# Kernel tuning notes

Measured on AMD Instinct MI355X. Metric: run time of the kernel, lower is better.

Reference implementation:

```python
import jax, jax.numpy as jnp
import numpy as np

ITER_N = 3  # iterNum
DIM = 256   # channel dim entering MPNCOV
# static flat indices of the upper triangle (row-major of dim*dim), as in Triuvec
_TRIU_I, _TRIU_J = np.triu_indices(DIM)
TRIU_IDX = jnp.asarray(_TRIU_I * DIM + _TRIU_J)


def setup_inputs() -> dict:
    key = jax.random.key(0)
    x = jax.random.normal(key, (256, 256, 14, 14), dtype=jnp.float32)
    return {"x": x}


def reference(x):
    B, C, H, W = x.shape
    M = H * W
    xr = x.reshape(B, C, M)
    # Covpool: y = x @ I_hat @ x^T with I_hat = (1/M)(I - (1/M) 1 1^T)
    # equivalently (1/M) * centered Gram matrix
    xc = xr - xr.mean(axis=2, keepdims=True)
    cov = jnp.einsum('bcm,bdm->bcd', xc, xc) / M  # [B, C, C]
    # Sqrtm: Newton-Schulz iteration (iSQRT-COV)
    I = jnp.eye(C, dtype=x.dtype)
    normA = jnp.trace(cov, axis1=1, axis2=2)  # = (1/3)*sum(cov * 3I)
    A = cov / normA[:, None, None]
    ZY = 0.5 * (3.0 * I - A)
    Yk = jnp.matmul(A, ZY)
    Zk = ZY
    for _ in range(ITER_N - 2):
        ZY = 0.5 * (3.0 * I - jnp.matmul(Zk, Yk))
        Yk = jnp.matmul(Yk, ZY)
        Zk = jnp.matmul(ZY, Zk)
    YZY = 0.5 * jnp.matmul(Yk, 3.0 * I - jnp.matmul(Zk, Yk))
    y = YZY * jnp.sqrt(normA)[:, None, None]
    # Triuvec: extract upper-triangular entries, [B, C*(C+1)/2]
    return y.reshape(B, C * C)[:, TRIU_IDX]
```

## Files before the change

### kernel.cpp

```cpp
#include <hip/hip_runtime.h>
#include <math.h>

#define BB 256
#define CC 256
#define MN 196
#define TRI 32896

#define MSC 32.0f
#define INV_MSC  (1.0f/32.0f)
#define INV_MSC2 (1.0f/1024.0f)

typedef _Float16 f16;
typedef f16   f16x8 __attribute__((ext_vector_type(8)));
typedef float f32x4 __attribute__((ext_vector_type(4)));
typedef unsigned u32x4 __attribute__((ext_vector_type(4)));

__device__ __forceinline__ unsigned pack_split(float v) {
    f16 h = (f16)v;
    f16 l = (f16)(v - (float)h);
    return (unsigned)__builtin_bit_cast(unsigned short, h) |
           ((unsigned)__builtin_bit_cast(unsigned short, l) << 16);
}
__device__ __forceinline__ float unpack_split(unsigned w) {
    f16 h = __builtin_bit_cast(f16, (unsigned short)(w & 0xffffu));
    f16 l = __builtin_bit_cast(f16, (unsigned short)(w >> 16));
    return (float)h + (float)l;
}
__device__ __forceinline__ f16x8 swap_pairs(f16x8 v) {
    return __builtin_shufflevector(v, v, 1, 0, 3, 2, 5, 4, 7, 6);
}
__device__ __forceinline__ void gload_lds16(const unsigned* g, const f16* l) {
    __builtin_amdgcn_global_load_lds(
        (__attribute__((address_space(1))) void*)(size_t)g,
        (__attribute__((address_space(3))) void*)(unsigned)(size_t)l,
        16, 0, 0);
}

__global__ __launch_bounds__(256) void xsplit_kernel(const float* __restrict__ x,
                                                     float* __restrict__ vr,
                                                     unsigned* __restrict__ xs, int b0) {
    int wave = (blockIdx.x * 256 + threadIdx.x) >> 6;
    int lane = threadIdx.x & 63;
    int bl = wave >> 8;
    int c  = wave & 255;
    int bg = b0 + bl;
    const float* row = x + ((size_t)bg * CC + c) * MN;
    float a0 = row[lane], a1 = row[lane + 64], a2 = row[lane + 128];
    float a3 = (lane < MN - 192) ? row[lane + 192] : 0.0f;
    float s = a0 + a1 + a2 + a3;
    float q = a0 * a0 + a1 * a1 + a2 * a2 + a3 * a3;
    #pragma unroll
    for (int off = 32; off > 0; off >>= 1) {
        s += __shfl_xor(s, off, 64);
        q += __shfl_xor(q, off, 64);
    }
    float m = s * (1.0f / MN);
    if (lane == 0) vr[bg * CC + c] = q * (1.0f / MN) - m * m;
    unsigned* orow = xs + ((size_t)bl * CC + c) * 256;
    orow[lane]       = pack_split(MSC * (a0 - m));
    orow[lane + 64]  = pack_split(MSC * (a1 - m));
    orow[lane + 128] = pack_split(MSC * (a2 - m));
    orow[lane + 192] = (lane < 4) ? pack_split(MSC * (a3 - m)) : 0u;
}

__global__ __launch_bounds__(256) void norm_kernel(const float* __restrict__ vr,
                                                   float* __restrict__ inv,
                                                   float* __restrict__ snorm,
                                                   float* __restrict__ invs, int b0) {
    __shared__ float red[256];
    int b = b0 + blockIdx.x, i = threadIdx.x;
    red[i] = vr[b * CC + i];
    __syncthreads();
    for (int s = 128; s > 0; s >>= 1) {
        if (i < s) red[i] += red[i + s];
        __syncthreads();
    }
    if (i == 0) {
        float n = red[0];
        inv[b] = 1.0f / n;
        float sq = sqrtf(n);
        snorm[b] = sq;
        invs[b] = 1.0f / sq;
    }
}

template <bool FINAL>
__global__ __launch_bounds__(256) void gemm256(const unsigned* __restrict__ Ag,
                                               const unsigned* __restrict__ Bg,
                                               const unsigned* __restrict__ Eg,
                                               void* __restrict__ Cg,
                                               const float alpha0, const float beta0,
                                               const float diag_add,
                                               const float* __restrict__ Sg, int b0) {
    __shared__ __align__(16) unsigned char smem[65536];

    int bid = blockIdx.x;
    const int nwg = gridDim.x;
    if ((nwg & 7) == 0) {
        const int cpx = nwg >> 3;
        bid = (bid & 7) * cpx + (bid >> 3);
    }
    const int bl = bid >> 2;
    const int t  = bid & 3;
    const int ti = t >> 1, tj = t & 1;
    if (FINAL && ti == 1 && tj == 0) return;
    const int bg = b0 + bl;
    const int tid  = threadIdx.x;
    const int lane = tid & 63;
    const int wid  = tid >> 6;
    const int wr = wid >> 1, wc = wid & 1;
    const int h = lane >> 4;
    const int d = lane & 15;

    const unsigned* Abase = Ag + (size_t)bl * (CC * CC) + (size_t)(ti * 128) * 256;
    const unsigned* Bbase = Bg + (size_t)bl * (CC * CC) + (size_t)(tj * 128) * 256;

    const unsigned* gpan = (wid < 2) ? Abase : Bbase;
    f16* lpan = (f16*)(smem + ((wid < 2) ? 0 : 32768));
    const int rbase = (wid & 1) * 64;
    const int sr = lane >> 3;
    const int sg = (lane & 7) ^ (lane >> 3);

    auto STAGE = [&](int nb, int ks) {
        #pragma unroll
        for (int i = 0; i < 8; ++i) {
            const unsigned* src = gpan + (size_t)(rbase + i * 8 + sr) * 256
                                       + ks * 32 + sg * 4;
            f16* dst = lpan + nb * 8192 + (rbase + i * 8) * 64;
            gload_lds16(src, dst);
        }
    };

    f32x4 acc[4][4];
    #pragma unroll
    for (int i = 0; i < 4; ++i)
        #pragma unroll
        for (int j = 0; j < 4; ++j) acc[i][j] = 0.0f;

    STAGE(0, 0);
    __syncthreads();
    #pragma unroll 1
    for (int ks = 0; ks < 8; ++ks) {
        const int nb = ks & 1;
        if (ks < 7) STAGE(nb ^ 1, ks + 1);
        #pragma unroll
        for (int kk = 0; kk < 2; ++kk) {
            const int swz = (((kk * 4 + h) ^ (d & 7)) << 4);
            f16x8 av[4], bv[4], bw[4];
            #pragma unroll
            for (int ib = 0; ib < 4; ++ib)
                av[ib] = *(const f16x8*)(smem + nb * 16384
                            + (wr * 64 + ib * 16 + d) * 128 + swz);
            #pragma unroll
            for (int jb = 0; jb < 4; ++jb) {
                bv[jb] = *(const f16x8*)(smem + 32768 + nb * 16384
                            + (wc * 64 + jb * 16 + d) * 128 + swz);
                bw[jb] = swap_pairs(bv[jb]);
            }
            #pragma unroll
            for (int ib = 0; ib < 4; ++ib)
                #pragma unroll
                for (int jb = 0; jb < 4; ++jb) {
                    acc[ib][jb] = __builtin_amdgcn_mfma_f32_16x16x32_f16(av[ib], bv[jb], acc[ib][jb], 0, 0, 0);
                    acc[ib][jb] = __builtin_amdgcn_mfma_f32_16x16x32_f16(av[ib], bw[jb], acc[ib][jb], 0, 0, 0);
                }
        }
        __syncthreads();
    }

    const int li0 = wr * 64 + h * 4;
    const int lj0 = wc * 64 + d;
    const int gi0 = ti * 128 + li0;
    const int gj0 = tj * 128 + lj0;
    unsigned* tile = (unsigned*)smem;

    if (!FINAL) {
        const float sc = (Sg != nullptr) ? Sg[bg] : 1.0f;
        const float al = alpha0 * sc;
        const float be = beta0 * sc;
        unsigned* Cb = (unsigned*)Cg + (size_t)bl * CC * CC;
        const unsigned* Eb = (Eg != nullptr) ? Eg + (size_t)bl * CC * CC : nullptr;

        if (Eb) {
            #pragma unroll
            for (int it = 0; it < 16; ++it) {
                int f = it * 256 + tid;
                int r = f >> 5, c4 = f & 31;
                *(u32x4*)&tile[r * 128 + c4 * 4] =
                    *(const u32x4*)&Eb[(size_t)(ti * 128 + r) * CC + tj * 128 + c4 * 4];
            }
            __syncthreads();
        }

        unsigned pk[4][4][4];
        #pragma unroll
        for (int ib = 0; ib < 4; ++ib)
            #pragma unroll
            for (int jb = 0; jb < 4; ++jb)
                #pragma unroll
                for (int q = 0; q < 4; ++q) {
                    int lr = li0 + ib * 16 + q;
                    int lc = lj0 + jb * 16;
                    float val = al * acc[ib][jb][q];
                    if (Eb) val += be * unpack_split(tile[lr * 128 + lc]);
                    if (gi0 + ib * 16 + q == gj0 + jb * 16) val += diag_add;
                    pk[ib][jb][q] = pack_split(val);
                }
        __syncthreads();

        #pragma unroll
        for (int ib = 0; ib < 4; ++ib)
            #pragma unroll
            for (int jb = 0; jb < 4; ++jb)
                #pragma unroll
                for (int q = 0; q < 4; ++q)
                    tile[(li0 + ib * 16 + q) * 128 + lj0 + jb * 16] = pk[ib][jb][q];
        __syncthreads();

        #pragma unroll
        for (int it = 0; it < 16; ++it) {
            int f = it * 256 + tid;
            int r = f >> 5, c4 = f & 31;
            *(u32x4*)&Cb[(size_t)(ti * 128 + r) * CC + tj * 128 + c4 * 4] =
                *(const u32x4*)&tile[r * 128 + c4 * 4];
        }
    } else {
        float* ob = (float*)Cg + (size_t)bg * TRI;
        #pragma unroll
        for (int ib = 0; ib < 4; ++ib)
            #pragma unroll
            for (int jb = 0; jb < 4; ++jb) {
                int gib = gi0 + ib * 16;
                int gj  = gj0 + jb * 16;
                #pragma unroll
                for (int q = 0; q < 4; ++q) {
                    int gi = gib + q;
                    if (gj >= gi)
                        ob[gi * CC - (gi * (gi - 1)) / 2 - gi + gj] = acc[ib][jb][q] * INV_MSC2;
                }
            }
    }
}

extern "C" void kernel_launch(void* const* d_in, const int* in_sizes, int n_in,
                              void* d_out, int out_size, void* d_ws, size_t ws_size,
                              hipStream_t stream) {
    const float* x = (const float*)d_in[0];
    float* out = (float*)d_out;
    unsigned* ws = (unsigned*)d_ws;

    const int SCR = BB * CC + 3 * BB;
    float* vr    = out + (out_size - SCR);
    float* inv   = vr + BB * CC;
    float* snorm = inv + BB;
    float* invs  = snorm + BB;

    size_t per_b = 4ull * CC * CC * sizeof(unsigned);
    int gmax = (int)(ws_size / per_b);
    int g = 1;
    while (g * 2 <= gmax && g * 2 <= BB) g *= 2;

    size_t slotf = (size_t)g * CC * CC;
    unsigned* s0 = ws;
    unsigned* s1 = ws + slotf;
    unsigned* s2 = ws + 2 * slotf;
    unsigned* s3 = ws + 3 * slotf;

    for (int b0 = 0; b0 < BB; b0 += g) {
        xsplit_kernel<<<g * 64, 256, 0, stream>>>(x, vr, s1, b0);
        norm_kernel<<<g, 256, 0, stream>>>(vr, inv, snorm, invs, b0);
        gemm256<false><<<g * 4, 256, 0, stream>>>(s1, s1, nullptr, (void*)s0,
                                                  1.0f / (MSC * MN), 0.0f, 0.0f, inv, b0);
        gemm256<false><<<g * 4, 256, 0, stream>>>(s0, s0, s0, (void*)s1, -0.5f * INV_MSC, 1.5f, 0.0f, nullptr, b0);
        gemm256<false><<<g * 4, 256, 0, stream>>>(s0, s1, s1, (void*)s2, 0.25f * INV_MSC, -0.75f, 1.5f * MSC, nullptr, b0);
        gemm256<false><<<g * 4, 256, 0, stream>>>(s1, s2, nullptr, (void*)s3, INV_MSC, 0.0f, 0.0f, snorm, b0);
        gemm256<false><<<g * 4, 256, 0, stream>>>(s2, s0, s2, (void*)s1, -0.5f * INV_MSC, 1.5f, 0.0f, invs, b0);
        gemm256<false><<<g * 4, 256, 0, stream>>>(s1, s3, nullptr, (void*)s0, -0.5f * INV_MSC, 0.0f, 1.5f * MSC, nullptr, b0);
        gemm256<true><<<g * 4, 256, 0, stream>>>(s3, s0, nullptr, d_out, 0.0f, 0.0f, 0.0f, nullptr, b0);
    }
}
```

Before: 400.1 us.

## Halve gemm LDS footprint with smaller K-stage and two-pass epilogue

Shared memory per block in the batched 256x256 split-fp16 GEMM drops from 64KB to 32KB. Each K stage now holds 16 columns instead of 32, so the loop runs 16 iterations with a new swizzle and precomputed LDS offsets. The epilogue writes its output tile in two 64-row halves, so the staging tile fits in the smaller buffer. The aim is more resident blocks per CU for better latency hiding, at the cost of twice as many barriers in the main loop and extra syncs in the epilogue.

```diff
diff --git a/kernel.cpp b/kernel.cpp
--- a/kernel.cpp
+++ b/kernel.cpp
@@ -29,7 +29,7 @@
 __device__ __forceinline__ f16x8 swap_pairs(f16x8 v) {
     return __builtin_shufflevector(v, v, 1, 0, 3, 2, 5, 4, 7, 6);
 }
-__device__ __forceinline__ void gload_lds16(const unsigned* g, const f16* l) {
+__device__ __forceinline__ void gload_lds16(const unsigned* g, const void* l) {
     __builtin_amdgcn_global_load_lds(
         (__attribute__((address_space(1))) void*)(size_t)g,
         (__attribute__((address_space(3))) void*)(unsigned)(size_t)l,
@@ -92,7 +92,7 @@
                                                const float alpha0, const float beta0,
                                                const float diag_add,
                                                const float* __restrict__ Sg, int b0) {
-    __shared__ __align__(16) unsigned char smem[65536];
+    __shared__ __align__(16) unsigned char smem[32768];
 
     int bid = blockIdx.x;
     const int nwg = gridDim.x;
@@ -116,20 +116,26 @@
     const unsigned* Bbase = Bg + (size_t)bl * (CC * CC) + (size_t)(tj * 128) * 256;
 
     const unsigned* gpan = (wid < 2) ? Abase : Bbase;
-    f16* lpan = (f16*)(smem + ((wid < 2) ? 0 : 32768));
+    const int lbank = (wid < 2) ? 0 : 16384;
     const int rbase = (wid & 1) * 64;
-    const int sr = lane >> 3;
-    const int sg = (lane & 7) ^ (lane >> 3);
+    const int sr = lane >> 2;
+    const int sg = (lane & 3) ^ ((lane >> 3) & 3);
+    const unsigned* gsl = gpan + (size_t)(rbase + sr) * 256 + (sg << 2);
 
     auto STAGE = [&](int nb, int ks) {
         #pragma unroll
-        for (int i = 0; i < 8; ++i) {
-            const unsigned* src = gpan + (size_t)(rbase + i * 8 + sr) * 256
-                                       + ks * 32 + sg * 4;
-            f16* dst = lpan + nb * 8192 + (rbase + i * 8) * 64;
-            gload_lds16(src, dst);
-        }
+        for (int i = 0; i < 4; ++i)
+            gload_lds16(gsl + (size_t)(i * 16) * 256 + ks * 16,
+                        smem + lbank + nb * 8192 + (rbase + i * 16) * 64);
     };
+
+    const int swz = ((h ^ ((d >> 1) & 3)) << 4);
+    int aoff[4], boff[4];
+    #pragma unroll
+    for (int ib = 0; ib < 4; ++ib) {
+        aoff[ib] = (wr * 64 + ib * 16 + d) * 64 + swz;
+        boff[ib] = 16384 + (wc * 64 + ib * 16 + d) * 64 + swz;
+    }
 
     f32x4 acc[4][4];
     #pragma unroll
@@ -140,31 +146,26 @@
     STAGE(0, 0);
     __syncthreads();
     #pragma unroll 1
-    for (int ks = 0; ks < 8; ++ks) {
+    for (int ks = 0; ks < 16; ++ks) {
         const int nb = ks & 1;
-        if (ks < 7) STAGE(nb ^ 1, ks + 1);
-        #pragma unroll
-        for (int kk = 0; kk < 2; ++kk) {
-            const int swz = (((kk * 4 + h) ^ (d & 7)) << 4);
-            f16x8 av[4], bv[4], bw[4];
-            #pragma unroll
-            for (int ib = 0; ib < 4; ++ib)
-                av[ib] = *(const f16x8*)(smem + nb * 16384
-                            + (wr * 64 + ib * 16 + d) * 128 + swz);
+        if (ks < 15) STAGE(nb ^ 1, ks + 1);
+        const char* base = (const char*)smem + nb * 8192;
+        f16x8 av[4], bv[4], bw[4];
+        #pragma unroll
+        for (int ib = 0; ib < 4; ++ib)
+            av[ib] = *(const f16x8*)(base + aoff[ib]);
+        #pragma unroll
+        for (int jb = 0; jb < 4; ++jb) {
+            bv[jb] = *(const f16x8*)(base + boff[jb]);
+            bw[jb] = swap_pairs(bv[jb]);
+        }
+        #pragma unroll
+        for (int ib = 0; ib < 4; ++ib)
             #pragma unroll
             for (int jb = 0; jb < 4; ++jb) {
-                bv[jb] = *(const f16x8*)(smem + 32768 + nb * 16384
-                            + (wc * 64 + jb * 16 + d) * 128 + swz);
-                bw[jb] = swap_pairs(bv[jb]);
-            }
-            #pragma unroll
-            for (int ib = 0; ib < 4; ++ib)
-                #pragma unroll
-                for (int jb = 0; jb < 4; ++jb) {
-                    acc[ib][jb] = __builtin_amdgcn_mfma_f32_16x16x32_f16(av[ib], bv[jb], acc[ib][jb], 0, 0, 0);
-                    acc[ib][jb] = __builtin_amdgcn_mfma_f32_16x16x32_f16(av[ib], bw[jb], acc[ib][jb], 0, 0, 0);
-                }
-        }
+                acc[ib][jb] = __builtin_amdgcn_mfma_f32_16x16x32_f16(av[ib], bv[jb], acc[ib][jb], 0, 0, 0);
+                acc[ib][jb] = __builtin_amdgcn_mfma_f32_16x16x32_f16(av[ib], bw[jb], acc[ib][jb], 0, 0, 0);
+            }
         __syncthreads();
     }
 
@@ -181,48 +182,42 @@
         unsigned* Cb = (unsigned*)Cg + (size_t)bl * CC * CC;
         const unsigned* Eb = (Eg != nullptr) ? Eg + (size_t)bl * CC * CC : nullptr;
 
-        if (Eb) {
+        #pragma unroll
+        for (int p = 0; p < 2; ++p) {
+            __syncthreads();
+            if (Eb) {
+                #pragma unroll
+                for (int it = 0; it < 8; ++it) {
+                    int f = it * 256 + tid;
+                    int r = f >> 5, c4 = f & 31;
+                    *(u32x4*)&tile[r * 128 + c4 * 4] =
+                        *(const u32x4*)&Eb[(size_t)(ti * 128 + p * 64 + r) * CC + tj * 128 + c4 * 4];
+                }
+            }
+            __syncthreads();
+            if (wr == p) {
+                #pragma unroll
+                for (int ib = 0; ib < 4; ++ib)
+                    #pragma unroll
+                    for (int jb = 0; jb < 4; ++jb)
+                        #pragma unroll
+                        for (int q = 0; q < 4; ++q) {
+                            int lr2 = h * 4 + ib * 16 + q;
+                            int lc  = lj0 + jb * 16;
+                            float val = al * acc[ib][jb][q];
+                            if (Eb) val += be * unpack_split(tile[lr2 * 128 + lc]);
+                            if (gi0 + ib * 16 + q == gj0 + jb * 16) val += diag_add;
+                            tile[lr2 * 128 + lc] = pack_split(val);
+                        }
+            }
+            __syncthreads();
             #pragma unroll
-            for (int it = 0; it < 16; ++it) {
+            for (int it = 0; it < 8; ++it) {
                 int f = it * 256 + tid;
                 int r = f >> 5, c4 = f & 31;
-                *(u32x4*)&tile[r * 128 + c4 * 4] =
-                    *(const u32x4*)&Eb[(size_t)(ti * 128 + r) * CC + tj * 128 + c4 * 4];
-            }
-            __syncthreads();
-        }
-
-        unsigned pk[4][4][4];
-        #pragma unroll
-        for (int ib = 0; ib < 4; ++ib)
-            #pragma unroll
-            for (int jb = 0; jb < 4; ++jb)
-                #pragma unroll
-                for (int q = 0; q < 4; ++q) {
-                    int lr = li0 + ib * 16 + q;
-                    int lc = lj0 + jb * 16;
-                    float val = al * acc[ib][jb][q];
-                    if (Eb) val += be * unpack_split(tile[lr * 128 + lc]);
-                    if (gi0 + ib * 16 + q == gj0 + jb * 16) val += diag_add;
-                    pk[ib][jb][q] = pack_split(val);
-                }
-        __syncthreads();
-
-        #pragma unroll
-        for (int ib = 0; ib < 4; ++ib)
-            #pragma unroll
-            for (int jb = 0; jb < 4; ++jb)
-                #pragma unroll
-                for (int q = 0; q < 4; ++q)
-                    tile[(li0 + ib * 16 + q) * 128 + lj0 + jb * 16] = pk[ib][jb][q];
-        __syncthreads();
-
-        #pragma unroll
-        for (int it = 0; it < 16; ++it) {
-            int f = it * 256 + tid;
-            int r = f >> 5, c4 = f & 31;
-            *(u32x4*)&Cb[(size_t)(ti * 128 + r) * CC + tj * 128 + c4 * 4] =
-                *(const u32x4*)&tile[r * 128 + c4 * 4];
+                *(u32x4*)&Cb[(size_t)(ti * 128 + p * 64 + r) * CC + tj * 128 + c4 * 4] =
+                    *(const u32x4*)&tile[r * 128 + c4 * 4];
+            }
         }
     } else {
         float* ob = (float*)Cg + (size_t)bg * TRI;
```

Result: slower. 451.6 us (+12.9%).
